# Kernel tuning notes

Hardware: AMD Instinct MI355X
Metric: run time of the kernel (lower is better)

Reference implementation:

```python
import jax, jax.numpy as jnp
import numpy as np

EPS = 1e-5
NUM_PIXELS = 2  # M_Relax window half-width


def _conv(x, w, b, groups=1, pad=0):
    y = jax.lax.conv_general_dilated(
        x, w, (1, 1), [(pad, pad), (pad, pad)],
        dimension_numbers=("NCHW", "OIHW", "NCHW"),
        feature_group_count=groups)
    return y + b[None, :, None, None]


def _bn(x, g, bta, m, v):
    # eval-mode BatchNorm2d with running stats
    inv = jax.lax.rsqrt(v + EPS)
    return g[None, :, None, None] * (x - m[None, :, None, None]) * inv[None, :, None, None] + bta[None, :, None, None]


def _resb(x, w1, b1, w2, b2):
    y = _conv(x, w1, b1, groups=4, pad=1)
    y = jnp.where(y > 0, y, 0.1 * y)  # LeakyReLU(0.1)
    y = _conv(y, w2, b2, groups=4, pad=1)
    return y + x


def _relax(M):
    # M: (N, w, w); sum of shifts +-NUM_PIXELS along the row (dim 1)
    w = M.shape[1]
    P = jnp.pad(M, ((0, 0), (NUM_PIXELS, NUM_PIXELS), (0, 0)))
    out = P[:, 0:w, :]
    for k in range(1, 2 * NUM_PIXELS + 1):
        out = out + P[:, k:k + w, :]
    return out


def setup_inputs() -> dict:
    key = jax.random.key(0)
    ks = jax.random.split(key, 16)
    b, c, h, w = 4, 64, 128, 256
    c2 = 2 * c
    s = 0.05
    inp = {
        "x_left": jax.random.normal(ks[0], (b, c, h, w), jnp.float32),
        "x_right": jax.random.normal(ks[1], (b, c, h, w), jnp.float32),
        "conv1_w": jax.random.normal(ks[2], (c, c, 1, 1), jnp.float32) * s,
        "conv1_b": jnp.zeros((c,), jnp.float32),
        "conv2_w": jax.random.normal(ks[3], (c, c, 1, 1), jnp.float32) * s,
        "conv2_b": jnp.zeros((c,), jnp.float32),
        "bn_g": jnp.ones((c2,), jnp.float32),
        "bn_b": jnp.zeros((c2,), jnp.float32),
        "bn_m": jax.random.normal(ks[4], (c2,), jnp.float32) * 0.1,
        "bn_v": jax.random.uniform(ks[5], (c2,), jnp.float32) + 0.5,
        "rb_w1": jax.random.normal(ks[6], (c2, c2 // 4, 3, 3), jnp.float32) * s,
        "rb_b1": jnp.zeros((c2,), jnp.float32),
        "rb_w2": jax.random.normal(ks[7], (c2, c2 // 4, 3, 3), jnp.float32) * s,
        "rb_b2": jnp.zeros((c2,), jnp.float32),
        "bq_w": jax.random.normal(ks[8], (c, c, 1, 1), jnp.float32) * s,
        "bq_b": jnp.zeros((c,), jnp.float32),
        "bs_w": jax.random.normal(ks[9], (c, c, 1, 1), jnp.float32) * s,
        "bs_b": jnp.zeros((c,), jnp.float32),
    }
    return inp


def reference(x_left, x_right, conv1_w, conv1_b, conv2_w, conv2_b,
              bn_g, bn_b, bn_m, bn_v, rb_w1, rb_b1, rb_w2, rb_b2,
              bq_w, bq_b, bs_w, bs_b):
    b, c, h, w = x_left.shape
    cat_l = jnp.concatenate([_conv(x_left, conv1_w, conv1_b), x_left], axis=1)
    cat_r = jnp.concatenate([_conv(x_right, conv2_w, conv2_b), x_right], axis=1)
    Q = _conv(_resb(_bn(cat_l, bn_g, bn_b, bn_m, bn_v), rb_w1, rb_b1, rb_w2, rb_b2), bq_w, bq_b, groups=2)
    K = _conv(_resb(_bn(cat_r, bn_g, bn_b, bn_m, bn_v), rb_w1, rb_b1, rb_w2, rb_b2), bs_w, bs_b, groups=2)
    Q = Q - Q.mean(axis=3, keepdims=True)
    K = K - K.mean(axis=3, keepdims=True)
    # score: (b*h, w, w) -- per-epipolar-row cross-view attention
    Qr = Q.transpose(0, 2, 3, 1).reshape(b * h, w, c)
    Kr = K.transpose(0, 2, 1, 3).reshape(b * h, c, w)
    score = jnp.matmul(Qr, Kr)
    M_r2l = jax.nn.softmax(score, axis=-1)
    M_l2r = jax.nn.softmax(score.transpose(0, 2, 1), axis=-1)
    # validity maps via relaxed cycle-consistency (detached in original)
    V_l = jnp.einsum("nij,nji->ni", _relax(M_r2l), M_l2r)
    V_r = jnp.einsum("nij,nji->ni", _relax(M_l2r), M_r2l)
    V_l = jax.lax.stop_gradient(V_l).reshape(b, 1, h, w)
    V_r = jax.lax.stop_gradient(V_r).reshape(b, 1, h, w)
    V_l_t = jnp.tanh(5.0 * V_l)
    V_r_t = jnp.tanh(5.0 * V_r)
    xl = x_left.transpose(0, 2, 3, 1).reshape(b * h, w, c)
    xr = x_right.transpose(0, 2, 3, 1).reshape(b * h, w, c)
    x_lT = jnp.matmul(M_r2l, xr).reshape(b, h, w, c).transpose(0, 3, 1, 2)
    x_rT = jnp.matmul(M_l2r, xl).reshape(b, h, w, c).transpose(0, 3, 1, 2)
    out_left = x_left * (1.0 - V_l_t) + x_lT * V_l_t
    out_right = x_right * (1.0 - V_r_t) + x_rT * V_r_t
    return out_left, out_right
```

## Files before the change

### kernel.cpp

```cpp
#include <hip/hip_runtime.h>
#include <math.h>

#define BB 4
#define CC 64
#define C2 128
#define HH 128
#define WW 256
#define NN (BB*HH)
#define EPSBN 1e-5f

typedef _Float16 f16;
typedef _Float16 half8 __attribute__((ext_vector_type(8)));
typedef float f32x4 __attribute__((ext_vector_type(4)));

__global__ __launch_bounds__(256) void k_wprep(
    const float* __restrict__ w1, const float* __restrict__ w2,
    f16* __restrict__ wp1, f16* __restrict__ wp2)
{
    int g = blockIdx.x; int which = blockIdx.y;
    const float* src = which ? w2 : w1;
    f16* dst = which ? wp2 : wp1;
    for (int p = threadIdx.x; p < 9216; p += 256) {
        int mo = p / 288; int kr = p - mo*288;
        int ks = kr >> 5; int ic = kr & 31;
        dst[g*9216 + p] = (f16)src[((g*32 + mo)*32 + ic)*9 + ks];
    }
}

__global__ __launch_bounds__(256) void k_catbn_m(
    const float* __restrict__ x, const float* __restrict__ cw, const float* __restrict__ cb,
    const float* __restrict__ g, const float* __restrict__ bb_, const float* __restrict__ m,
    const float* __restrict__ v, f16* __restrict__ u)
{
    __shared__ f16 Xl[256][72];
    __shared__ f16 Wl[64][72];
    __shared__ float sS[64], sT[64], sS2[64], sT2[64];
    int n = blockIdx.x; int b = n >> 7; int h = n & 127; int t = threadIdx.x;
    for (int p = t; p < 2048; p += 256) {
        int idx = p * 2; int o = idx >> 6, i = idx & 63;
        union { f16 h[2]; unsigned int u1; } pr;
        pr.h[0] = (f16)cw[idx]; pr.h[1] = (f16)cw[idx + 1];
        *(unsigned int*)&Wl[o][i] = pr.u1;
    }
    if (t < 64) {
        float inv = rsqrtf(v[t] + EPSBN); float s = g[t] * inv;
        sS[t] = s; sT[t] = bb_[t] + s * (cb[t] - m[t]);
        float inv2 = rsqrtf(v[t + 64] + EPSBN); float s2 = g[t + 64] * inv2;
        sS2[t] = s2; sT2[t] = bb_[t + 64] - s2 * m[t + 64];
    }
    __syncthreads();
    f16* up = u + ((size_t)(n*256 + t)) * 128;
    for (int c8 = 0; c8 < 8; ++c8) {
        float xv8[8];
#pragma unroll
        for (int j = 0; j < 8; ++j)
            xv8[j] = x[(((b*64 + c8*8 + j)*128 + h) << 8) + t];
        union { f16 h[8]; uint4 v4; } pk;
#pragma unroll
        for (int j = 0; j < 8; ++j) {
            int c = c8*8 + j;
            pk.h[j] = (f16)(sS2[c]*xv8[j] + sT2[c]);
        }
        *(uint4*)(up + 64 + c8*8) = pk.v4;
#pragma unroll
        for (int j2 = 0; j2 < 4; ++j2) {
            union { f16 h[2]; unsigned int u1; } q;
            q.h[0] = (f16)xv8[j2*2]; q.h[1] = (f16)xv8[j2*2 + 1];
            *(unsigned int*)&Xl[t][c8*8 + j2*2] = q.u1;
        }
    }
    __syncthreads();
    int lane = t & 63, wv = t >> 6;
    int m16 = lane & 15, quad = lane >> 4;
    half8 af[4][2], bf[4][2];
#pragma unroll
    for (int mt = 0; mt < 4; ++mt)
#pragma unroll
        for (int kk = 0; kk < 2; ++kk)
            af[mt][kk] = *(const half8*)&Wl[mt*16 + m16][kk*32 + quad*8];
#pragma unroll
    for (int nt = 0; nt < 4; ++nt)
#pragma unroll
        for (int kk = 0; kk < 2; ++kk)
            bf[nt][kk] = *(const half8*)&Xl[wv*64 + nt*16 + m16][kk*32 + quad*8];
    f32x4 acc[4][4] = {};
#pragma unroll
    for (int mt = 0; mt < 4; ++mt)
#pragma unroll
        for (int nt = 0; nt < 4; ++nt) {
            acc[mt][nt] = __builtin_amdgcn_mfma_f32_16x16x32_f16(af[mt][0], bf[nt][0], acc[mt][nt], 0, 0, 0);
            acc[mt][nt] = __builtin_amdgcn_mfma_f32_16x16x32_f16(af[mt][1], bf[nt][1], acc[mt][nt], 0, 0, 0);
        }
#pragma unroll
    for (int mt = 0; mt < 4; ++mt) {
        int ocb = mt*16 + quad*4;
        float s4[4], t4[4];
        *(float4*)s4 = *(const float4*)&sS[ocb];
        *(float4*)t4 = *(const float4*)&sT[ocb];
#pragma unroll
        for (int nt = 0; nt < 4; ++nt) {
            int px = wv*64 + nt*16 + m16;
            union { f16 h[4]; uint2 u2; } ov;
#pragma unroll
            for (int r = 0; r < 4; ++r)
                ov.h[r] = (f16)(s4[r]*acc[mt][nt][r] + t4[r]);
            *(uint2*)(u + ((size_t)(n*256 + px))*128 + ocb) = ov.u2;
        }
    }
}

template<bool LEAKY, bool RES>
__global__ __launch_bounds__(256, 2) void k_conv3r(
    const f16* __restrict__ in, const f16* __restrict__ wp,
    const float* __restrict__ bias, const f16* __restrict__ res,
    f16* __restrict__ out)
{
    __shared__ f16 Xl[6*130*40];
    int b = blockIdx.x >> 5; int h0 = (blockIdx.x & 31) * 4;
    int g = blockIdx.y; int w0 = blockIdx.z * 128;
    int t = threadIdx.x;
    int lane = t & 63, wv = t >> 6;
    int m16 = lane & 15, quad = lane >> 4;
    const f16* wg = wp + g*9216;
    half8 af[2][9];
#pragma unroll
    for (int mt = 0; mt < 2; ++mt)
#pragma unroll
        for (int ks = 0; ks < 9; ++ks)
            af[mt][ks] = *(const half8*)(wg + (mt*16 + m16)*288 + ks*32 + quad*8);
    float bo[2][4];
#pragma unroll
    for (int mt = 0; mt < 2; ++mt)
#pragma unroll
        for (int r = 0; r < 4; ++r)
            bo[mt][r] = bias[g*32 + mt*16 + quad*4 + r];
    for (int idx = t; idx < 3120; idx += 256) {
        int r = idx / 520; int rem = idx - r*520; int p = rem >> 2; int q = rem & 3;
        int hr = h0 + r - 1; int wg2 = w0 + p - 1;
        uint4 val = make_uint4(0,0,0,0);
        if ((unsigned)wg2 < 256u && (unsigned)hr < 128u)
            val = *(const uint4*)(in + ((size_t)((b*128 + hr)*256 + wg2))*128 + g*32 + q*8);
        *(uint4*)&Xl[(r*130 + p)*40 + q*8] = val;
    }
    __syncthreads();
    int px0 = wv*32 + m16;
#pragma unroll
    for (int rr = 0; rr < 4; ++rr) {
        f32x4 acc[2][2] = {};
#pragma unroll
        for (int ks = 0; ks < 9; ++ks) {
            int ky = ks / 3, kx = ks - ky*3;
            half8 bf0 = *(const half8*)&Xl[((rr + ky)*130 + px0 + kx)*40 + quad*8];
            half8 bf1 = *(const half8*)&Xl[((rr + ky)*130 + px0 + 16 + kx)*40 + quad*8];
            acc[0][0] = __builtin_amdgcn_mfma_f32_16x16x32_f16(af[0][ks], bf0, acc[0][0], 0, 0, 0);
            acc[0][1] = __builtin_amdgcn_mfma_f32_16x16x32_f16(af[0][ks], bf1, acc[0][1], 0, 0, 0);
            acc[1][0] = __builtin_amdgcn_mfma_f32_16x16x32_f16(af[1][ks], bf0, acc[1][0], 0, 0, 0);
            acc[1][1] = __builtin_amdgcn_mfma_f32_16x16x32_f16(af[1][ks], bf1, acc[1][1], 0, 0, 0);
        }
        int h = h0 + rr;
#pragma unroll
        for (int mt = 0; mt < 2; ++mt)
#pragma unroll
            for (int nt = 0; nt < 2; ++nt) {
                int px = w0 + wv*32 + nt*16 + m16;
                int oc = g*32 + mt*16 + quad*4;
                size_t off = ((size_t)((b*128 + h)*256 + px))*128 + oc;
                float rv4[4] = {0.f, 0.f, 0.f, 0.f};
                if (RES) {
                    union { f16 h[4]; uint2 v2; } rrd;
                    rrd.v2 = *(const uint2*)(res + off);
#pragma unroll
                    for (int r = 0; r < 4; ++r) rv4[r] = (float)rrd.h[r];
                }
                union { f16 h[4]; uint2 v2; } ov;
#pragma unroll
                for (int r = 0; r < 4; ++r) {
                    float y = acc[mt][nt][r] + bo[mt][r];
                    if (LEAKY) y = y > 0.f ? y : 0.1f*y;
                    if (RES) y += rv4[r];
                    ov.h[r] = (f16)y;
                }
                *(uint2*)(out + off) = ov.v2;
            }
    }
}

__global__ __launch_bounds__(256, 2) void k_conv1x1m(
    const f16* __restrict__ in, const float* __restrict__ wgt,
    f16* __restrict__ outq)
{
    __shared__ f16 Xl[256][72];
    __shared__ f16 Wl[64][72];
    __shared__ float partial[4][64];
    __shared__ float meanS[64];
    int n = blockIdx.x; int t = threadIdx.x;
    int lane = t & 63, wv = t >> 6;
    int m16 = lane & 15, quad = lane >> 4;
    for (int p = t; p < 2048; p += 256) {
        int idx = p * 2; int o = idx >> 6, i = idx & 63;
        union { f16 h[2]; unsigned int u1; } pr;
        pr.h[0] = (f16)wgt[idx]; pr.h[1] = (f16)wgt[idx + 1];
        *(unsigned int*)&Wl[o][i] = pr.u1;
    }
    f32x4 acc[4][4] = {};
    const f16* rp = in + ((size_t)n*256 + t)*128;
    for (int g = 0; g < 2; ++g) {
#pragma unroll
        for (int i8 = 0; i8 < 8; ++i8)
            *(uint4*)&Xl[t][i8*8] = *(const uint4*)(rp + g*64 + i8*8);
        __syncthreads();
        half8 af[2][2], bf[4][2];
#pragma unroll
        for (int ml = 0; ml < 2; ++ml)
#pragma unroll
            for (int kk = 0; kk < 2; ++kk)
                af[ml][kk] = *(const half8*)&Wl[g*32 + ml*16 + m16][kk*32 + quad*8];
#pragma unroll
        for (int nt = 0; nt < 4; ++nt)
#pragma unroll
            for (int kk = 0; kk < 2; ++kk)
                bf[nt][kk] = *(const half8*)&Xl[wv*64 + nt*16 + m16][kk*32 + quad*8];
#pragma unroll
        for (int ml = 0; ml < 2; ++ml)
#pragma unroll
            for (int nt = 0; nt < 4; ++nt) {
                int mt = g*2 + ml;
                acc[mt][nt] = __builtin_amdgcn_mfma_f32_16x16x32_f16(af[ml][0], bf[nt][0], acc[mt][nt], 0, 0, 0);
                acc[mt][nt] = __builtin_amdgcn_mfma_f32_16x16x32_f16(af[ml][1], bf[nt][1], acc[mt][nt], 0, 0, 0);
            }
        __syncthreads();
    }
#pragma unroll
    for (int mt = 0; mt < 4; ++mt)
#pragma unroll
        for (int r = 0; r < 4; ++r) {
            float s = acc[mt][0][r] + acc[mt][1][r] + acc[mt][2][r] + acc[mt][3][r];
            s += __shfl_xor(s, 1); s += __shfl_xor(s, 2);
            s += __shfl_xor(s, 4); s += __shfl_xor(s, 8);
            if (m16 == 0) partial[wv][mt*16 + quad*4 + r] = s;
        }
    __syncthreads();
    if (t < 64)
        meanS[t] = (partial[0][t] + partial[1][t] + partial[2][t] + partial[3][t]) * (1.0f/256.0f);
    __syncthreads();
    f16* qp = outq + ((size_t)n*256)*64;
#pragma unroll
    for (int mt = 0; mt < 4; ++mt) {
        int ocb = mt*16 + quad*4;
        float m4[4]; *(float4*)m4 = *(const float4*)&meanS[ocb];
#pragma unroll
        for (int nt = 0; nt < 4; ++nt) {
            int px = wv*64 + nt*16 + m16;
            union { f16 h[4]; uint2 u2; } ov;
#pragma unroll
            for (int r = 0; r < 4; ++r)
                ov.h[r] = (f16)(acc[mt][nt][r] - m4[r]);
            *(uint2*)(qp + (size_t)px*64 + ocb) = ov.u2;
        }
    }
}

__global__ __launch_bounds__(256) void k_score(
    const f16* __restrict__ Q, const f16* __restrict__ K,
    f16* __restrict__ S, f16* __restrict__ ST)
{
    __shared__ f16 Qs[256][72];
    __shared__ f16 Ks[64][72];
    int n = blockIdx.x; int t = threadIdx.x;
    const f16* qg = Q + (size_t)n*16384 + (size_t)t*64;
#pragma unroll
    for (int k = 0; k < 8; ++k)
        *(uint4*)&Qs[t][k*8] = *(const uint4*)(qg + k*8);
    int lane = t & 63, wv = t >> 6;
    int m16 = lane & 15, quad = lane >> 4;
    int m0 = wv*64;
    half8 af[4][2];
    bool afl = false;
    f16* Sn = S + (size_t)n*65536;
    f16* STn = ST + (size_t)n*65536;
    for (int jc = 0; jc < 256; jc += 64) {
        __syncthreads();
        {
            int jj = t >> 2, seg = (t & 3) * 16;
            const f16* kg = K + (size_t)n*16384 + (size_t)(jc + jj)*64 + seg;
            *(uint4*)&Ks[jj][seg]     = *(const uint4*)(kg);
            *(uint4*)&Ks[jj][seg + 8] = *(const uint4*)(kg + 8);
        }
        __syncthreads();
        if (!afl) {
            afl = true;
#pragma unroll
            for (int mt = 0; mt < 4; ++mt)
#pragma unroll
                for (int kk = 0; kk < 2; ++kk)
                    af[mt][kk] = *(const half8*)&Qs[m0 + mt*16 + m16][kk*32 + quad*8];
        }
        half8 bf[4][2];
#pragma unroll
        for (int nt = 0; nt < 4; ++nt)
#pragma unroll
            for (int kk = 0; kk < 2; ++kk)
                bf[nt][kk] = *(const half8*)&Ks[nt*16 + m16][kk*32 + quad*8];
        f32x4 acc[4][4] = {};
#pragma unroll
        for (int mt = 0; mt < 4; ++mt)
#pragma unroll
            for (int nt = 0; nt < 4; ++nt) {
                acc[mt][nt] = __builtin_amdgcn_mfma_f32_16x16x32_f16(af[mt][0], bf[nt][0], acc[mt][nt], 0, 0, 0);
                acc[mt][nt] = __builtin_amdgcn_mfma_f32_16x16x32_f16(af[mt][1], bf[nt][1], acc[mt][nt], 0, 0, 0);
            }
#pragma unroll
        for (int mt = 0; mt < 4; ++mt)
#pragma unroll
            for (int nt = 0; nt < 4; ++nt) {
                int i = m0 + mt*16 + quad*4;
                int j = jc + nt*16 + m16;
                union { f16 h[4]; uint2 u2; } pv;
#pragma unroll
                for (int r = 0; r < 4; ++r) {
                    f16 vv = (f16)acc[mt][nt][r];
                    Sn[(size_t)(i + r)*256 + j] = vv;
                    pv.h[r] = vv;
                }
                *(uint2*)&STn[(size_t)j*256 + i] = pv.u2;
            }
    }
}

__global__ __launch_bounds__(256) void k_stats(
    const f16* __restrict__ S, float* __restrict__ rmax, float* __restrict__ rsumi,
    float* __restrict__ cmax, float* __restrict__ csumi)
{
    __shared__ float CM[8][260], CS[8][260];
    int n = blockIdx.x, t = threadIdx.x;
    int rphase = t >> 5;
    int c0 = (t & 31) * 8;
    const f16* Sp = S + (size_t)n*65536;
    float colm[8], cols[8];
#pragma unroll
    for (int e = 0; e < 8; ++e) { colm[e] = -1e30f; cols[e] = 0.f; }
    for (int g = 0; g < 32; ++g) {
        int row = g*8 + rphase;
        union { uint4 v4; f16 h[8]; } ld;
        ld.v4 = *(const uint4*)(Sp + (size_t)row*256 + c0);
        float v[8];
#pragma unroll
        for (int e = 0; e < 8; ++e) v[e] = (float)ld.h[e];
        float mx = v[0];
#pragma unroll
        for (int e = 1; e < 8; ++e) mx = fmaxf(mx, v[e]);
#pragma unroll
        for (int off = 1; off < 32; off <<= 1) mx = fmaxf(mx, __shfl_xor(mx, off));
        float es = 0.f;
#pragma unroll
        for (int e = 0; e < 8; ++e) es += __expf(v[e] - mx);
#pragma unroll
        for (int off = 1; off < 32; off <<= 1) es += __shfl_xor(es, off);
        if ((t & 31) == 0) { rmax[n*256 + row] = mx; rsumi[n*256 + row] = 1.0f/es; }
#pragma unroll
        for (int e = 0; e < 8; ++e) {
            float nm = fmaxf(colm[e], v[e]);
            cols[e] = cols[e]*__expf(colm[e] - nm) + __expf(v[e] - nm);
            colm[e] = nm;
        }
    }
#pragma unroll
    for (int e = 0; e < 8; ++e) { CM[rphase][c0 + e] = colm[e]; CS[rphase][c0 + e] = cols[e]; }
    __syncthreads();
    float m = CM[0][t], s = CS[0][t];
#pragma unroll
    for (int gp = 1; gp < 8; ++gp) {
        float m2 = CM[gp][t], s2 = CS[gp][t];
        float nm = fmaxf(m, m2);
        s = s*__expf(m - nm) + s2*__expf(m2 - nm);
        m = nm;
    }
    cmax[n*256 + t] = m;
    csumi[n*256 + t] = 1.0f/s;
}

__global__ __launch_bounds__(256) void k_out(
    const f16* __restrict__ P16, const float* __restrict__ sm, const float* __restrict__ si,
    const float* __restrict__ om, const float* __restrict__ oi,
    const float* __restrict__ xB, const float* __restrict__ xP,
    float* __restrict__ outp)
{
    __shared__ f16 Pl[260][72];
    __shared__ f16 Xl[64][72];
    __shared__ float cmS[256], ciS[256];
    __shared__ float Vs[256];
    int n = blockIdx.x; int b = n >> 7; int h = n & 127;
    int t = threadIdx.x;
    int lane = t & 63, wv = t >> 6;
    int m16 = lane & 15, quad = lane >> 4;
    if (t < 18)      *(uint4*)(&Pl[0][0]   + t*8)      = make_uint4(0,0,0,0);
    else if (t < 36) *(uint4*)(&Pl[258][0] + (t-18)*8) = make_uint4(0,0,0,0);
    cmS[t] = om[n*256 + t];
    ciS[t] = oi[n*256 + t];
    float rm = sm[n*256 + t], ri = si[n*256 + t];
    f32x4 acc[4][4] = {};
    float vacc = 0.f;
    for (int kc = 0; kc < 256; kc += 64) {
        uint4 raw8[8];
        const f16* pg = P16 + (size_t)n*65536 + (size_t)t*256 + kc;
#pragma unroll
        for (int k8 = 0; k8 < 8; ++k8) {
            union { uint4 v4; f16 h[8]; } ldu, stu;
            ldu.v4 = *(const uint4*)(pg + k8*8);
            raw8[k8] = ldu.v4;
#pragma unroll
            for (int e = 0; e < 8; ++e)
                stu.h[e] = (f16)(__expf((float)ldu.h[e] - rm) * ri);
            *(uint4*)&Pl[t + 2][k8*8] = stu.v4;
        }
        {
            int c = t >> 2, j0 = (t & 3) * 16;
            const float* xg = xB + (((size_t)(b*64 + c)*128 + h) << 8) + kc + j0;
            union { uint4 v4; f16 h[8]; } xu0, xu1;
#pragma unroll
            for (int e = 0; e < 8; ++e) xu0.h[e] = (f16)xg[e];
#pragma unroll
            for (int e = 0; e < 8; ++e) xu1.h[e] = (f16)xg[8 + e];
            *(uint4*)&Xl[c][j0]     = xu0.v4;
            *(uint4*)&Xl[c][j0 + 8] = xu1.v4;
        }
        __syncthreads();
        int mbase = wv*64;
        half8 a0[4][2], b0[4][2];
#pragma unroll
        for (int mt = 0; mt < 4; ++mt)
#pragma unroll
            for (int kk = 0; kk < 2; ++kk)
                a0[mt][kk] = *(const half8*)&Pl[mbase + mt*16 + m16 + 2][kk*32 + quad*8];
#pragma unroll
        for (int nt = 0; nt < 4; ++nt)
#pragma unroll
            for (int kk = 0; kk < 2; ++kk)
                b0[nt][kk] = *(const half8*)&Xl[nt*16 + m16][kk*32 + quad*8];
#pragma unroll
        for (int mt = 0; mt < 4; ++mt)
#pragma unroll
            for (int nt = 0; nt < 4; ++nt) {
                acc[mt][nt] = __builtin_amdgcn_mfma_f32_16x16x32_f16(a0[mt][0], b0[nt][0], acc[mt][nt], 0, 0, 0);
                acc[mt][nt] = __builtin_amdgcn_mfma_f32_16x16x32_f16(a0[mt][1], b0[nt][1], acc[mt][nt], 0, 0, 0);
            }
#pragma unroll
        for (int j8 = 0; j8 < 8; ++j8) {
            int jl = j8*8;
            half8 w0 = *(const half8*)&Pl[t + 0][jl];
            half8 w1 = *(const half8*)&Pl[t + 1][jl];
            half8 w2 = *(const half8*)&Pl[t + 2][jl];
            half8 w3 = *(const half8*)&Pl[t + 3][jl];
            half8 w4 = *(const half8*)&Pl[t + 4][jl];
            half8 win = w0 + w1 + w2 + w3 + w4;
            union { uint4 v4; f16 h[8]; } rw; rw.v4 = raw8[j8];
#pragma unroll
            for (int e = 0; e < 8; ++e) {
                int j = kc + jl + e;
                float Bv = __expf((float)rw.h[e] - cmS[j]) * ciS[j];
                vacc = fmaf((float)win[e], Bv, vacc);
            }
        }
        __syncthreads();
    }
    Vs[t] = vacc;
    __syncthreads();
#pragma unroll
    for (int mt = 0; mt < 4; ++mt) {
        int i0 = wv*64 + mt*16 + quad*4;
        float v4[4];
        *(float4*)v4 = *(const float4*)&Vs[i0];
        float tv[4];
#pragma unroll
        for (int r = 0; r < 4; ++r) tv[r] = tanhf(5.f*v4[r]);
#pragma unroll
        for (int nt = 0; nt < 4; ++nt) {
            int c = nt*16 + m16;
            size_t base = (((size_t)(b*64 + c)*128 + h) << 8) + i0;
            float xp4[4]; *(float4*)xp4 = *(const float4*)&xP[base];
            float o4[4];
#pragma unroll
            for (int r = 0; r < 4; ++r)
                o4[r] = xp4[r]*(1.f - tv[r]) + acc[mt][nt][r]*tv[r];
            *(float4*)&outp[base] = *(float4*)o4;
        }
    }
}

extern "C" void kernel_launch(void* const* d_in, const int* in_sizes, int n_in,
                              void* d_out, int out_size, void* d_ws, size_t ws_size,
                              hipStream_t stream)
{
    const float* x_left  = (const float*)d_in[0];
    const float* x_right = (const float*)d_in[1];
    const float* conv1_w = (const float*)d_in[2];
    const float* conv1_b = (const float*)d_in[3];
    const float* conv2_w = (const float*)d_in[4];
    const float* conv2_b = (const float*)d_in[5];
    const float* bn_g    = (const float*)d_in[6];
    const float* bn_b    = (const float*)d_in[7];
    const float* bn_m    = (const float*)d_in[8];
    const float* bn_v    = (const float*)d_in[9];
    const float* rb_w1   = (const float*)d_in[10];
    const float* rb_b1   = (const float*)d_in[11];
    const float* rb_w2   = (const float*)d_in[12];
    const float* rb_b2   = (const float*)d_in[13];
    const float* bq_w    = (const float*)d_in[14];
    const float* bs_w    = (const float*)d_in[16];

    f16* W16 = (f16*)d_ws;
    f16* u  = W16;
    f16* y1 = W16 + 16777216;
    f16* r  = W16 + 33554432;
    f16* S  = W16;
    f16* ST = W16 + 33554432;
    f16* Qh = W16 + 67108864;
    f16* Kh = W16 + 75497472;
    float* F32  = (float*)(W16 + 83886080);
    float* rmax  = F32;
    float* rsumi = F32 + 131072;
    float* cmax  = F32 + 262144;
    float* csumi = F32 + 393216;
    f16* Wp1 = W16 + 84934656;
    f16* Wp2 = W16 + 84971520;

    float* out_left  = (float*)d_out;
    float* out_right = (float*)d_out + 8388608;

    k_wprep<<<dim3(4, 2), 256, 0, stream>>>(rb_w1, rb_w2, Wp1, Wp2);

    k_catbn_m<<<NN, 256, 0, stream>>>(x_left, conv1_w, conv1_b, bn_g, bn_b, bn_m, bn_v, u);
    k_conv3r<true,  false><<<dim3(128, 4, 2), 256, 0, stream>>>(u, Wp1, rb_b1, nullptr, y1);
    k_conv3r<false, true ><<<dim3(128, 4, 2), 256, 0, stream>>>(y1, Wp2, rb_b2, u, r);
    k_conv1x1m<<<NN, 256, 0, stream>>>(r, bq_w, Qh);

    k_catbn_m<<<NN, 256, 0, stream>>>(x_right, conv2_w, conv2_b, bn_g, bn_b, bn_m, bn_v, u);
    k_conv3r<true,  false><<<dim3(128, 4, 2), 256, 0, stream>>>(u, Wp1, rb_b1, nullptr, y1);
    k_conv3r<false, true ><<<dim3(128, 4, 2), 256, 0, stream>>>(y1, Wp2, rb_b2, u, r);
    k_conv1x1m<<<NN, 256, 0, stream>>>(r, bs_w, Kh);

    k_score<<<NN, 256, 0, stream>>>(Qh, Kh, S, ST);
    k_stats<<<NN, 256, 0, stream>>>(S, rmax, rsumi, cmax, csumi);
    k_out<<<NN, 256, 0, stream>>>(S,  rmax, rsumi, cmax, csumi, x_right, x_left,  out_left);
    k_out<<<NN, 256, 0, stream>>>(ST, cmax, csumi, rmax, rsumi, x_left,  x_right, out_right);
}
```

Baseline: 515.9 us.

## Fuse score, softmax stats and output into one LDS-resident attention kernel

Replaces the score, stats and two output kernels with one 512-thread kernel per row. It computes the 256x256 score tile in swizzled LDS, derives row and column softmax stats from LDS, then does the relax/validity pass and the P·X MFMA from the same tile. The transposed view is handled by calling the kernel again with Q and K swapped, which recomputes the score instead of writing S and ST to global memory. This removes large global f16 score traffic and several launches, at the cost of 128KB+ LDS (one block per CU), duplicated score matmuls and serial column reductions.

```diff
diff --git a/kernel.cpp b/kernel.cpp
--- a/kernel.cpp
+++ b/kernel.cpp
@@ -260,219 +260,176 @@
     }
 }
 
-__global__ __launch_bounds__(256) void k_score(
-    const f16* __restrict__ Q, const f16* __restrict__ K,
-    f16* __restrict__ S, f16* __restrict__ ST)
-{
-    __shared__ f16 Qs[256][72];
-    __shared__ f16 Ks[64][72];
-    int n = blockIdx.x; int t = threadIdx.x;
-    const f16* qg = Q + (size_t)n*16384 + (size_t)t*64;
-#pragma unroll
-    for (int k = 0; k < 8; ++k)
-        *(uint4*)&Qs[t][k*8] = *(const uint4*)(qg + k*8);
-    int lane = t & 63, wv = t >> 6;
-    int m16 = lane & 15, quad = lane >> 4;
-    int m0 = wv*64;
-    half8 af[4][2];
-    bool afl = false;
-    f16* Sn = S + (size_t)n*65536;
-    f16* STn = ST + (size_t)n*65536;
-    for (int jc = 0; jc < 256; jc += 64) {
-        __syncthreads();
-        {
-            int jj = t >> 2, seg = (t & 3) * 16;
-            const f16* kg = K + (size_t)n*16384 + (size_t)(jc + jj)*64 + seg;
-            *(uint4*)&Ks[jj][seg]     = *(const uint4*)(kg);
-            *(uint4*)&Ks[jj][seg + 8] = *(const uint4*)(kg + 8);
-        }
-        __syncthreads();
-        if (!afl) {
-            afl = true;
-#pragma unroll
-            for (int mt = 0; mt < 4; ++mt)
-#pragma unroll
-                for (int kk = 0; kk < 2; ++kk)
-                    af[mt][kk] = *(const half8*)&Qs[m0 + mt*16 + m16][kk*32 + quad*8];
-        }
-        half8 bf[4][2];
-#pragma unroll
-        for (int nt = 0; nt < 4; ++nt)
-#pragma unroll
-            for (int kk = 0; kk < 2; ++kk)
-                bf[nt][kk] = *(const half8*)&Ks[nt*16 + m16][kk*32 + quad*8];
-        f32x4 acc[4][4] = {};
-#pragma unroll
-        for (int mt = 0; mt < 4; ++mt)
-#pragma unroll
-            for (int nt = 0; nt < 4; ++nt) {
-                acc[mt][nt] = __builtin_amdgcn_mfma_f32_16x16x32_f16(af[mt][0], bf[nt][0], acc[mt][nt], 0, 0, 0);
-                acc[mt][nt] = __builtin_amdgcn_mfma_f32_16x16x32_f16(af[mt][1], bf[nt][1], acc[mt][nt], 0, 0, 0);
-            }
-#pragma unroll
-        for (int mt = 0; mt < 4; ++mt)
-#pragma unroll
-            for (int nt = 0; nt < 4; ++nt) {
-                int i = m0 + mt*16 + quad*4;
-                int j = jc + nt*16 + m16;
-                union { f16 h[4]; uint2 u2; } pv;
-#pragma unroll
-                for (int r = 0; r < 4; ++r) {
-                    f16 vv = (f16)acc[mt][nt][r];
-                    Sn[(size_t)(i + r)*256 + j] = vv;
-                    pv.h[r] = vv;
-                }
-                *(uint2*)&STn[(size_t)j*256 + i] = pv.u2;
-            }
-    }
-}
-
-__global__ __launch_bounds__(256) void k_stats(
-    const f16* __restrict__ S, float* __restrict__ rmax, float* __restrict__ rsumi,
-    float* __restrict__ cmax, float* __restrict__ csumi)
-{
-    __shared__ float CM[8][260], CS[8][260];
-    int n = blockIdx.x, t = threadIdx.x;
-    int rphase = t >> 5;
-    int c0 = (t & 31) * 8;
-    const f16* Sp = S + (size_t)n*65536;
-    float colm[8], cols[8];
-#pragma unroll
-    for (int e = 0; e < 8; ++e) { colm[e] = -1e30f; cols[e] = 0.f; }
-    for (int g = 0; g < 32; ++g) {
-        int row = g*8 + rphase;
-        union { uint4 v4; f16 h[8]; } ld;
-        ld.v4 = *(const uint4*)(Sp + (size_t)row*256 + c0);
-        float v[8];
-#pragma unroll
-        for (int e = 0; e < 8; ++e) v[e] = (float)ld.h[e];
-        float mx = v[0];
-#pragma unroll
-        for (int e = 1; e < 8; ++e) mx = fmaxf(mx, v[e]);
-#pragma unroll
-        for (int off = 1; off < 32; off <<= 1) mx = fmaxf(mx, __shfl_xor(mx, off));
-        float es = 0.f;
-#pragma unroll
-        for (int e = 0; e < 8; ++e) es += __expf(v[e] - mx);
-#pragma unroll
-        for (int off = 1; off < 32; off <<= 1) es += __shfl_xor(es, off);
-        if ((t & 31) == 0) { rmax[n*256 + row] = mx; rsumi[n*256 + row] = 1.0f/es; }
-#pragma unroll
-        for (int e = 0; e < 8; ++e) {
-            float nm = fmaxf(colm[e], v[e]);
-            cols[e] = cols[e]*__expf(colm[e] - nm) + __expf(v[e] - nm);
-            colm[e] = nm;
-        }
-    }
-#pragma unroll
-    for (int e = 0; e < 8; ++e) { CM[rphase][c0 + e] = colm[e]; CS[rphase][c0 + e] = cols[e]; }
-    __syncthreads();
-    float m = CM[0][t], s = CS[0][t];
-#pragma unroll
-    for (int gp = 1; gp < 8; ++gp) {
-        float m2 = CM[gp][t], s2 = CS[gp][t];
-        float nm = fmaxf(m, m2);
-        s = s*__expf(m - nm) + s2*__expf(m2 - nm);
-        m = nm;
-    }
-    cmax[n*256 + t] = m;
-    csumi[n*256 + t] = 1.0f/s;
-}
-
-__global__ __launch_bounds__(256) void k_out(
-    const f16* __restrict__ P16, const float* __restrict__ sm, const float* __restrict__ si,
-    const float* __restrict__ om, const float* __restrict__ oi,
+__global__ __launch_bounds__(512, 1) void k_attn(
+    const f16* __restrict__ Aq, const f16* __restrict__ Bk,
     const float* __restrict__ xB, const float* __restrict__ xP,
     float* __restrict__ outp)
 {
-    __shared__ f16 Pl[260][72];
-    __shared__ f16 Xl[64][72];
-    __shared__ float cmS[256], ciS[256];
-    __shared__ float Vs[256];
+    __shared__ f16 Sl[65536];
+    __shared__ f16 Pl[260][40];
+    __shared__ f16 Xl[64][40];
+    __shared__ float rmS[256], riS[256], cmS[256], ciS[256];
+    __shared__ float scr[2][256];
     int n = blockIdx.x; int b = n >> 7; int h = n & 127;
     int t = threadIdx.x;
     int lane = t & 63, wv = t >> 6;
     int m16 = lane & 15, quad = lane >> 4;
-    if (t < 18)      *(uint4*)(&Pl[0][0]   + t*8)      = make_uint4(0,0,0,0);
-    else if (t < 36) *(uint4*)(&Pl[258][0] + (t-18)*8) = make_uint4(0,0,0,0);
-    cmS[t] = om[n*256 + t];
-    ciS[t] = oi[n*256 + t];
-    float rm = sm[n*256 + t], ri = si[n*256 + t];
-    f32x4 acc[4][4] = {};
+    int W = wv * 32;
+
+    const f16* ag = Aq + (size_t)n*16384;
+    const f16* bg = Bk + (size_t)n*16384;
+    half8 af1[2][2];
+#pragma unroll
+    for (int mt = 0; mt < 2; ++mt)
+#pragma unroll
+        for (int kk = 0; kk < 2; ++kk)
+            af1[mt][kk] = *(const half8*)(ag + (size_t)(W + mt*16 + m16)*64 + kk*32 + quad*8);
+    for (int jc = 0; jc < 256; jc += 64) {
+        half8 bf1[4][2];
+#pragma unroll
+        for (int nt = 0; nt < 4; ++nt)
+#pragma unroll
+            for (int kk = 0; kk < 2; ++kk)
+                bf1[nt][kk] = *(const half8*)(bg + (size_t)(jc + nt*16 + m16)*64 + kk*32 + quad*8);
+        f32x4 acc1[2][4] = {};
+#pragma unroll
+        for (int mt = 0; mt < 2; ++mt)
+#pragma unroll
+            for (int nt = 0; nt < 4; ++nt) {
+                acc1[mt][nt] = __builtin_amdgcn_mfma_f32_16x16x32_f16(af1[mt][0], bf1[nt][0], acc1[mt][nt], 0, 0, 0);
+                acc1[mt][nt] = __builtin_amdgcn_mfma_f32_16x16x32_f16(af1[mt][1], bf1[nt][1], acc1[mt][nt], 0, 0, 0);
+            }
+#pragma unroll
+        for (int mt = 0; mt < 2; ++mt)
+#pragma unroll
+            for (int nt = 0; nt < 4; ++nt)
+#pragma unroll
+                for (int r = 0; r < 4; ++r) {
+                    int row = W + mt*16 + quad*4 + r;
+                    int col = jc + nt*16 + m16;
+                    int byte = (row << 9) + ((col*2) ^ ((row & 7) << 4));
+                    *(f16*)((char*)Sl + byte) = (f16)acc1[mt][nt][r];
+                }
+    }
+    __syncthreads();
+
+    if (t < 256) {
+        int r = t; int xo = (r & 7) << 4;
+        const char* base = (const char*)Sl + (r << 9);
+        float m = -1e30f;
+#pragma unroll 4
+        for (int g = 0; g < 32; ++g) {
+            half8 v8 = *(const half8*)(base + ((g*16) ^ xo));
+#pragma unroll
+            for (int e = 0; e < 8; ++e) m = fmaxf(m, (float)v8[e]);
+        }
+        float s = 0.f;
+#pragma unroll 4
+        for (int g = 0; g < 32; ++g) {
+            half8 v8 = *(const half8*)(base + ((g*16) ^ xo));
+#pragma unroll
+            for (int e = 0; e < 8; ++e) s += __expf((float)v8[e] - m);
+        }
+        rmS[r] = m; riS[r] = 1.0f/s;
+    } else {
+        int c = t - 256; int c2 = c*2;
+        const char* base = (const char*)Sl;
+        float m = -1e30f;
+#pragma unroll 8
+        for (int row = 0; row < 256; ++row) {
+            f16 v = *(const f16*)(base + (row << 9) + (c2 ^ ((row & 7) << 4)));
+            m = fmaxf(m, (float)v);
+        }
+        float s = 0.f;
+#pragma unroll 8
+        for (int row = 0; row < 256; ++row) {
+            f16 v = *(const f16*)(base + (row << 9) + (c2 ^ ((row & 7) << 4)));
+            s += __expf((float)v - m);
+        }
+        cmS[c] = m; ciS[c] = 1.0f/s;
+    }
+    if (t < 10)       *(uint4*)((char*)&Pl[0][0]   + t*16)      = make_uint4(0,0,0,0);
+    else if (t < 20)  *(uint4*)((char*)&Pl[258][0] + (t-10)*16) = make_uint4(0,0,0,0);
+    __syncthreads();
+
+    int r = t & 255, hc = t >> 8;
+    int cbase = hc * 16;
+    float rm = rmS[r], ri = riS[r];
+    int xc = t >> 3, xj = (t & 7) * 4;
+    const float* xg = xB + ((size_t)(b*64 + xc)*128 + h)*256;
+    f32x4 acc[2][4] = {};
     float vacc = 0.f;
-    for (int kc = 0; kc < 256; kc += 64) {
-        uint4 raw8[8];
-        const f16* pg = P16 + (size_t)n*65536 + (size_t)t*256 + kc;
-#pragma unroll
-        for (int k8 = 0; k8 < 8; ++k8) {
-            union { uint4 v4; f16 h[8]; } ldu, stu;
-            ldu.v4 = *(const uint4*)(pg + k8*8);
-            raw8[k8] = ldu.v4;
-#pragma unroll
-            for (int e = 0; e < 8; ++e)
-                stu.h[e] = (f16)(__expf((float)ldu.h[e] - rm) * ri);
-            *(uint4*)&Pl[t + 2][k8*8] = stu.v4;
-        }
+    const char* sb = (const char*)Sl + (r << 9);
+    int xo = (r & 7) << 4;
+    for (int kc = 0; kc < 256; kc += 32) {
+        float sraw[16];
         {
-            int c = t >> 2, j0 = (t & 3) * 16;
-            const float* xg = xB + (((size_t)(b*64 + c)*128 + h) << 8) + kc + j0;
-            union { uint4 v4; f16 h[8]; } xu0, xu1;
-#pragma unroll
-            for (int e = 0; e < 8; ++e) xu0.h[e] = (f16)xg[e];
-#pragma unroll
-            for (int e = 0; e < 8; ++e) xu1.h[e] = (f16)xg[8 + e];
-            *(uint4*)&Xl[c][j0]     = xu0.v4;
-            *(uint4*)&Xl[c][j0 + 8] = xu1.v4;
+            half8 v0 = *(const half8*)(sb + ((((kc + cbase)*2))      ^ xo));
+            half8 v1 = *(const half8*)(sb + ((((kc + cbase)*2) + 16) ^ xo));
+            half8 p0, p1;
+#pragma unroll
+            for (int e = 0; e < 8; ++e) {
+                sraw[e] = (float)v0[e];
+                p0[e] = (f16)(__expf(sraw[e] - rm) * ri);
+            }
+#pragma unroll
+            for (int e = 0; e < 8; ++e) {
+                sraw[8 + e] = (float)v1[e];
+                p1[e] = (f16)(__expf(sraw[8 + e] - rm) * ri);
+            }
+            char* pb = (char*)&Pl[r + 2][cbase];
+            *(half8*)pb = p0; *(half8*)(pb + 16) = p1;
+        }
+        {
+            float4 x4 = *(const float4*)(xg + kc + xj);
+            union { f16 h[4]; uint2 v2; } px;
+            px.h[0] = (f16)x4.x; px.h[1] = (f16)x4.y;
+            px.h[2] = (f16)x4.z; px.h[3] = (f16)x4.w;
+            *(uint2*)&Xl[xc][xj] = px.v2;
         }
         __syncthreads();
-        int mbase = wv*64;
-        half8 a0[4][2], b0[4][2];
-#pragma unroll
-        for (int mt = 0; mt < 4; ++mt)
-#pragma unroll
-            for (int kk = 0; kk < 2; ++kk)
-                a0[mt][kk] = *(const half8*)&Pl[mbase + mt*16 + m16 + 2][kk*32 + quad*8];
+#pragma unroll
+        for (int j8 = 0; j8 < 2; ++j8) {
+            const char* wb = (const char*)&Pl[r][cbase + j8*8];
+            half8 w0 = *(const half8*)(wb);
+            half8 w1 = *(const half8*)(wb + 80);
+            half8 w2 = *(const half8*)(wb + 160);
+            half8 w3 = *(const half8*)(wb + 240);
+            half8 w4 = *(const half8*)(wb + 320);
+            half8 win = w0 + w1 + w2 + w3 + w4;
+#pragma unroll
+            for (int e = 0; e < 8; ++e) {
+                int j = kc + cbase + j8*8 + e;
+                float Bv = __expf(sraw[j8*8 + e] - cmS[j]) * ciS[j];
+                vacc = fmaf((float)win[e], Bv, vacc);
+            }
+        }
+        half8 pa[2], xb_[4];
+#pragma unroll
+        for (int mt = 0; mt < 2; ++mt)
+            pa[mt] = *(const half8*)((const char*)&Pl[W + mt*16 + m16 + 2][0] + quad*16);
 #pragma unroll
         for (int nt = 0; nt < 4; ++nt)
-#pragma unroll
-            for (int kk = 0; kk < 2; ++kk)
-                b0[nt][kk] = *(const half8*)&Xl[nt*16 + m16][kk*32 + quad*8];
-#pragma unroll
-        for (int mt = 0; mt < 4; ++mt)
-#pragma unroll
-            for (int nt = 0; nt < 4; ++nt) {
-                acc[mt][nt] = __builtin_amdgcn_mfma_f32_16x16x32_f16(a0[mt][0], b0[nt][0], acc[mt][nt], 0, 0, 0);
-                acc[mt][nt] = __builtin_amdgcn_mfma_f32_16x16x32_f16(a0[mt][1], b0[nt][1], acc[mt][nt], 0, 0, 0);
-            }
-#pragma unroll
-        for (int j8 = 0; j8 < 8; ++j8) {
-            int jl = j8*8;
-            half8 w0 = *(const half8*)&Pl[t + 0][jl];
-            half8 w1 = *(const half8*)&Pl[t + 1][jl];
-            half8 w2 = *(const half8*)&Pl[t + 2][jl];
-            half8 w3 = *(const half8*)&Pl[t + 3][jl];
-            half8 w4 = *(const half8*)&Pl[t + 4][jl];
-            half8 win = w0 + w1 + w2 + w3 + w4;
-            union { uint4 v4; f16 h[8]; } rw; rw.v4 = raw8[j8];
-#pragma unroll
-            for (int e = 0; e < 8; ++e) {
-                int j = kc + jl + e;
-                float Bv = __expf((float)rw.h[e] - cmS[j]) * ciS[j];
-                vacc = fmaf((float)win[e], Bv, vacc);
-            }
-        }
+            xb_[nt] = *(const half8*)((const char*)&Xl[nt*16 + m16][0] + quad*16);
+#pragma unroll
+        for (int mt = 0; mt < 2; ++mt)
+#pragma unroll
+            for (int nt = 0; nt < 4; ++nt)
+                acc[mt][nt] = __builtin_amdgcn_mfma_f32_16x16x32_f16(pa[mt], xb_[nt], acc[mt][nt], 0, 0, 0);
         __syncthreads();
     }
-    Vs[t] = vacc;
-    __syncthreads();
-#pragma unroll
-    for (int mt = 0; mt < 4; ++mt) {
-        int i0 = wv*64 + mt*16 + quad*4;
+    scr[hc][r] = vacc;
+    __syncthreads();
+    if (t < 256) rmS[t] = scr[0][t] + scr[1][t];
+    __syncthreads();
+#pragma unroll
+    for (int mt = 0; mt < 2; ++mt) {
+        int i0 = W + mt*16 + quad*4;
         float v4[4];
-        *(float4*)v4 = *(const float4*)&Vs[i0];
+        *(float4*)v4 = *(const float4*)&rmS[i0];
         float tv[4];
 #pragma unroll
-        for (int r = 0; r < 4; ++r) tv[r] = tanhf(5.f*v4[r]);
+        for (int rr = 0; rr < 4; ++rr) tv[rr] = tanhf(5.f*v4[rr]);
 #pragma unroll
         for (int nt = 0; nt < 4; ++nt) {
             int c = nt*16 + m16;
@@ -480,8 +437,8 @@
             float xp4[4]; *(float4*)xp4 = *(const float4*)&xP[base];
             float o4[4];
 #pragma unroll
-            for (int r = 0; r < 4; ++r)
-                o4[r] = xp4[r]*(1.f - tv[r]) + acc[mt][nt][r]*tv[r];
+            for (int rr = 0; rr < 4; ++rr)
+                o4[rr] = xp4[rr]*(1.f - tv[rr]) + acc[mt][nt][rr]*tv[rr];
             *(float4*)&outp[base] = *(float4*)o4;
         }
     }
@@ -512,15 +469,8 @@
     f16* u  = W16;
     f16* y1 = W16 + 16777216;
     f16* r  = W16 + 33554432;
-    f16* S  = W16;
-    f16* ST = W16 + 33554432;
     f16* Qh = W16 + 67108864;
     f16* Kh = W16 + 75497472;
-    float* F32  = (float*)(W16 + 83886080);
-    float* rmax  = F32;
-    float* rsumi = F32 + 131072;
-    float* cmax  = F32 + 262144;
-    float* csumi = F32 + 393216;
     f16* Wp1 = W16 + 84934656;
     f16* Wp2 = W16 + 84971520;
 
@@ -539,8 +489,6 @@
     k_conv3r<false, true ><<<dim3(128, 4, 2), 256, 0, stream>>>(y1, Wp2, rb_b2, u, r);
     k_conv1x1m<<<NN, 256, 0, stream>>>(r, bs_w, Kh);
 
-    k_score<<<NN, 256, 0, stream>>>(Qh, Kh, S, ST);
-    k_stats<<<NN, 256, 0, stream>>>(S, rmax, rsumi, cmax, csumi);
-    k_out<<<NN, 256, 0, stream>>>(S,  rmax, rsumi, cmax, csumi, x_right, x_left,  out_left);
-    k_out<<<NN, 256, 0, stream>>>(ST, cmax, csumi, rmax, rsumi, x_left,  x_right, out_right);
-}
+    k_attn<<<NN, 512, 0, stream>>>(Qh, Kh, x_right, x_left,  out_left);
+    k_attn<<<NN, 512, 0, stream>>>(Kh, Qh, x_left,  x_right, out_right);
+}
```

After: 520.6 us. Within noise of the previous version (+0.9%).
